# Kernel optimization log

Hardware: AMD Instinct MI355X
Metric: run time of the kernel (lower is better)

Reference implementation:

```python
import jax, jax.numpy as jnp
import numpy as np

B, S, D, E = 8, 2048, 1024, 8
TOKENS = B * S
CAPACITY = TOKENS // E  # capacity_factor=1.0, top-1 gating (deepspeed default)


def _moe_layer(x_flat, Wg, We, be):
    """DeepSpeed-style top-1 MoE: gate -> capacity drop -> dispatch -> expert GEMM -> combine.
    x_flat: [T, D]; Wg: [D, E]; We: [E, D, D]; be: [E, D]."""
    gates = jax.nn.softmax(x_flat @ Wg, axis=-1)              # [T, E]
    idx = jnp.argmax(gates, axis=1)                            # [T] expert per token
    mask = jax.nn.one_hot(idx, E, dtype=jnp.int32)             # [T, E]
    loc = jnp.cumsum(mask, axis=0) - 1                         # position within expert
    loc_s = jnp.sum(loc * mask, axis=1)                        # [T]
    keep = loc_s < CAPACITY                                    # capacity drop
    gate_s = jnp.sum(gates * mask.astype(gates.dtype), axis=1) * keep.astype(gates.dtype)
    slot = jnp.clip(loc_s, 0, CAPACITY - 1)
    # dispatch: scatter kept tokens into [E, C, D] buffer (slots are unique for kept tokens)
    disp = jnp.zeros((E, CAPACITY, D), x_flat.dtype).at[idx, slot].add(
        x_flat * keep[:, None].astype(x_flat.dtype))
    # grouped expert GEMM
    eo = jnp.einsum('ecd,edf->ecf', disp, We) + be[:, None, :]  # [E, C, D]
    # combine: gather each token's expert output, scale by its gate value
    return eo[idx, slot] * gate_s[:, None]                      # [T, D]


def reference(x, y, W1, b1, Wg2, We2, be2, Wg3, We3, be3):
    h = jnp.einsum('bsd,df->bsf', x, W1) + b1                  # dense pre-layer
    hf = h.reshape(TOKENS, D)
    o = _moe_layer(hf, Wg2, We2, be2)
    o = _moe_layer(o, Wg3, We3, be3)
    h = h + o.reshape(B, S, D)                                 # residual add
    sent = h.mean(axis=1)                                      # [B, D]
    logp = jax.nn.log_softmax(sent, axis=-1)
    return -jnp.mean(logp[jnp.arange(B), y])                   # CrossEntropyLoss


def setup_inputs() -> dict:
    key = jax.random.key(0)
    ks = jax.random.split(key, 10)
    s = 0.02
    return {
        'x': jax.random.normal(ks[0], (B, S, D), jnp.float32),
        'y': jax.random.randint(ks[1], (B,), 0, D),
        'W1': jax.random.normal(ks[2], (D, D), jnp.float32) * s,
        'b1': jnp.zeros((D,), jnp.float32),
        'Wg2': jax.random.normal(ks[3], (D, E), jnp.float32) * s,
        'We2': jax.random.normal(ks[4], (E, D, D), jnp.float32) * s,
        'be2': jnp.zeros((E, D), jnp.float32),
        'Wg3': jax.random.normal(ks[5], (D, E), jnp.float32) * s,
        'We3': jax.random.normal(ks[6], (E, D, D), jnp.float32) * s,
        'be3': jnp.zeros((E, D), jnp.float32),
    }
```

## Files before the change

### kernel.cpp

```cpp
#include <hip/hip_runtime.h>
#include <hip/hip_bf16.h>
#include <math.h>


#define TOKS 16384
#define DIM 1024
#define NEXP 8
#define CAP 2048
#define BATCH 8
#define SEQ 2048

typedef __bf16 bf16_t;
typedef __bf16 bf16x8 __attribute__((ext_vector_type(8)));
typedef float fx4 __attribute__((ext_vector_type(4)));

__device__ __forceinline__ void gll16(const bf16_t* g, bf16_t* l) {
  __builtin_amdgcn_global_load_lds(
      (const __attribute__((address_space(1))) unsigned int*)g,
      (__attribute__((address_space(3))) unsigned int*)l, 16, 0, 0);
}

__global__ __launch_bounds__(256) void k_prep_w(
    const float* __restrict__ W1, const float* __restrict__ We2,
    const float* __restrict__ We3, bf16_t* __restrict__ Wt) {
  __shared__ float t[64][65];
  const int m = blockIdx.z;
  const float* src = (m == 0) ? W1
                     : (m <= 8) ? We2 + (size_t)(m - 1) * DIM * DIM
                                : We3 + (size_t)(m - 9) * DIM * DIM;
  bf16_t* dst = Wt + (size_t)m * DIM * DIM;
  const int n0 = blockIdx.x * 64, k0 = blockIdx.y * 64;
  const int tid = threadIdx.x;
  const int r = tid >> 4, c4 = (tid & 15) * 4;
#pragma unroll
  for (int i = 0; i < 4; i++) {
    float4 v = *(const float4*)&src[(size_t)(k0 + i * 16 + r) * DIM + n0 + c4];
    t[i * 16 + r][c4] = v.x;
    t[i * 16 + r][c4 + 1] = v.y;
    t[i * 16 + r][c4 + 2] = v.z;
    t[i * 16 + r][c4 + 3] = v.w;
  }
  __syncthreads();
#pragma unroll
  for (int i = 0; i < 4; i++) {
    int rn = i * 16 + r;
    union { bf16_t b[4]; uint2 u; } tmp;
#pragma unroll
    for (int j = 0; j < 4; j++) tmp.b[j] = (bf16_t)t[c4 + j][rn];
    *(uint2*)&dst[(size_t)(n0 + rn) * DIM + k0 + c4] = tmp.u;
  }
}

__global__ __launch_bounds__(256) void k_prep_wg(
    const float* __restrict__ Wg2, const float* __restrict__ Wg3,
    bf16_t* __restrict__ WgP) {
  const int which = blockIdx.x;
  const float* src = which ? Wg3 : Wg2;
  bf16_t* dst = WgP + which * (128 * 8 * 8);
  const int tid = threadIdx.x;
#pragma unroll
  for (int j = 0; j < 4; j++) {
    int d = tid * 4 + j;
    float4 a = *(const float4*)&src[d * 8];
    float4 b = *(const float4*)&src[d * 8 + 4];
    float v[8] = {a.x, a.y, a.z, a.w, b.x, b.y, b.z, b.w};
#pragma unroll
    for (int e = 0; e < 8; e++)
      dst[((d >> 3) * 8 + e) * 8 + (d & 7)] = (bf16_t)v[e];
  }
}

__global__ __launch_bounds__(256) void k_cvt_x(const float* __restrict__ x,
                                               bf16_t* __restrict__ xb) {
  size_t i = ((size_t)blockIdx.x * 256 + threadIdx.x) * 8;
  float4 a = *(const float4*)&x[i];
  float4 b = *(const float4*)&x[i + 4];
  union { bf16_t h[8]; uint4 u; } t;
  t.h[0] = (bf16_t)a.x; t.h[1] = (bf16_t)a.y; t.h[2] = (bf16_t)a.z; t.h[3] = (bf16_t)a.w;
  t.h[4] = (bf16_t)b.x; t.h[5] = (bf16_t)b.y; t.h[6] = (bf16_t)b.z; t.h[7] = (bf16_t)b.w;
  *(uint4*)&xb[i] = t.u;
}

__global__ __launch_bounds__(256) void k_gemm_dense(
    const bf16_t* __restrict__ A, const bf16_t* __restrict__ Bt,
    const float* __restrict__ bias, bf16_t* __restrict__ out) {
  __shared__ alignas(16) bf16_t As[128 * 64];
  __shared__ alignas(16) bf16_t Bs[128 * 64];
  const int tid = threadIdx.x;
  const int lane = tid & 63, wave = tid >> 6;
  const int quad = lane >> 4, l15 = lane & 15;
  const int wr = (wave >> 1) * 64, wc = (wave & 1) * 64;
  const int id = blockIdx.x;
  const int j_ = id >> 3;
  const int m0 = ((id & 7) * 16 + (j_ >> 3)) * 128;
  const int n0 = (j_ & 7) * 128;
  const int kc = (tid & 7) ^ ((tid >> 3) & 7);
  const int rbase = tid >> 3;

  const bf16_t* gA[4];
  const bf16_t* gB[4];
  bf16_t* lA[4];
  bf16_t* lB[4];
#pragma unroll
  for (int i = 0; i < 4; i++) {
    int r = rbase + 32 * i;
    gA[i] = A + (size_t)(m0 + r) * DIM + kc * 8;
    gB[i] = Bt + (size_t)(n0 + r) * DIM + kc * 8;
    lA[i] = &As[(wave * 64 + 256 * i) * 8];
    lB[i] = &Bs[(wave * 64 + 256 * i) * 8];
  }

  fx4 acc[4][4];
#pragma unroll
  for (int i = 0; i < 4; i++)
#pragma unroll
    for (int j = 0; j < 4; j++) acc[i][j] = (fx4)0.0f;

  for (int k0 = 0; k0 < DIM; k0 += 64) {
#pragma unroll
    for (int i = 0; i < 4; i++) gll16(gA[i] + k0, lA[i]);
#pragma unroll
    for (int i = 0; i < 4; i++) gll16(gB[i] + k0, lB[i]);
    __syncthreads();
#pragma unroll
    for (int s = 0; s < 2; s++) {
      const int pofs = ((s * 4 + quad) ^ (l15 & 7)) << 3;
      bf16x8 av[4], bv[4];
#pragma unroll
      for (int i = 0; i < 4; i++)
        av[i] = *(const bf16x8*)&As[(wr + i * 16 + l15) * 64 + pofs];
#pragma unroll
      for (int j = 0; j < 4; j++)
        bv[j] = *(const bf16x8*)&Bs[(wc + j * 16 + l15) * 64 + pofs];
#pragma unroll
      for (int i = 0; i < 4; i++)
#pragma unroll
        for (int j = 0; j < 4; j++)
          acc[i][j] = __builtin_amdgcn_mfma_f32_16x16x32_bf16(av[i], bv[j], acc[i][j], 0, 0, 0);
    }
    __syncthreads();
  }
#pragma unroll
  for (int j = 0; j < 4; j++) {
    int col = n0 + wc + j * 16 + l15;
    float bb = bias[col];
#pragma unroll
    for (int i = 0; i < 4; i++)
#pragma unroll
      for (int r = 0; r < 4; r++) {
        int m = m0 + wr + i * 16 + quad * 4 + r;
        out[(size_t)m * DIM + col] = (bf16_t)(acc[i][j][r] + bb);
      }
  }
}

__global__ __launch_bounds__(256) void k_gate_mm(
    const bf16_t* __restrict__ act, const bf16_t* __restrict__ WgP,
    int* __restrict__ idx, float* __restrict__ gate) {
  __shared__ alignas(16) bf16_t As[64 * 64];
  __shared__ alignas(16) bf16_t WgS[128 * 64];
  __shared__ float L[64][8];
  const int tid = threadIdx.x;
  const int lane = tid & 63, wave = tid >> 6;
  const int quad = lane >> 4, l15 = lane & 15;
  const int m0 = blockIdx.x * 64;
  const int kc = (tid & 7) ^ ((tid >> 3) & 7);
  const int rbase = tid >> 3;

#pragma unroll
  for (int j = 0; j < 4; j++)
    gll16(WgP + (j * 256 + wave * 64 + lane) * 8,
          &WgS[(j * 256 + wave * 64) * 8]);

  const bf16_t* gA[2];
  bf16_t* lA[2];
#pragma unroll
  for (int i = 0; i < 2; i++) {
    gA[i] = act + (size_t)(m0 + rbase + 32 * i) * DIM + kc * 8;
    lA[i] = &As[wave * 512 + i * 2048];
  }

  fx4 acc = (fx4)0.0f;
  for (int k0 = 0; k0 < DIM; k0 += 64) {
#pragma unroll
    for (int i = 0; i < 2; i++) gll16(gA[i] + k0, lA[i]);
    __syncthreads();
#pragma unroll
    for (int s = 0; s < 2; s++) {
      const int pofs = ((s * 4 + quad) ^ (l15 & 7)) << 3;
      bf16x8 av = *(const bf16x8*)&As[(wave * 16 + l15) * 64 + pofs];
      bf16x8 bv = *(const bf16x8*)&WgS[((k0 >> 3) + s * 4 + quad) * 64 + (l15 & 7) * 8];
      acc = __builtin_amdgcn_mfma_f32_16x16x32_bf16(av, bv, acc, 0, 0, 0);
    }
    __syncthreads();
  }
  if (l15 < 8) {
#pragma unroll
    for (int r = 0; r < 4; r++) L[wave * 16 + quad * 4 + r][l15] = acc[r];
  }
  __syncthreads();
  if (tid < 64) {
    float lg[8];
#pragma unroll
    for (int e = 0; e < 8; e++) lg[e] = L[tid][e];
    float best = lg[0];
    int bi = 0;
#pragma unroll
    for (int e = 1; e < 8; e++)
      if (lg[e] > best) { best = lg[e]; bi = e; }
    float s = 0.f;
#pragma unroll
    for (int e = 0; e < 8; e++) s += expf(lg[e] - best);
    idx[m0 + tid] = bi;
    gate[m0 + tid] = 1.0f / s;
  }
}

__global__ __launch_bounds__(1024) void k_route(
    const int* __restrict__ idx, int* __restrict__ tok, int* __restrict__ cnt,
    int* __restrict__ drop, int* __restrict__ ndrop) {
  const int e = blockIdx.x;
  const int tid = threadIdx.x, lane = tid & 63, wv = tid >> 6;
  __shared__ int wsum[16];
  const int4* p = (const int4*)(idx + tid * 16);
  int m[16];
  int c = 0;
#pragma unroll
  for (int j = 0; j < 4; j++) {
    int4 v = p[j];
    m[j * 4 + 0] = (v.x == e);
    m[j * 4 + 1] = (v.y == e);
    m[j * 4 + 2] = (v.z == e);
    m[j * 4 + 3] = (v.w == e);
    c += m[j * 4] + m[j * 4 + 1] + m[j * 4 + 2] + m[j * 4 + 3];
  }
  int sc = c;
#pragma unroll
  for (int off = 1; off < 64; off <<= 1) {
    int n = __shfl_up(sc, off);
    if (lane >= off) sc += n;
  }
  if (lane == 63) wsum[wv] = sc;
  __syncthreads();
  int wb = 0, tot = 0;
#pragma unroll
  for (int i = 0; i < 16; i++) {
    int s = wsum[i];
    tot += s;
    if (i < wv) wb += s;
  }
  int pos = wb + sc - c;
#pragma unroll
  for (int j = 0; j < 16; j++) {
    if (m[j]) {
      if (pos < CAP) {
        tok[e * CAP + pos] = tid * 16 + j;
      } else {
        int di = atomicAdd(ndrop, 1);
        drop[di] = tid * 16 + j;
      }
      pos++;
    }
  }
  if (tid == 0) cnt[e] = tot < CAP ? tot : CAP;
}

__global__ __launch_bounds__(128) void k_zero_rows(
    bf16_t* __restrict__ buf, const int* __restrict__ drop,
    const int* __restrict__ ndrop) {
  const int nd = *ndrop;
  const uint4 z = {0u, 0u, 0u, 0u};
  for (int j = blockIdx.x; j < nd; j += gridDim.x) {
    int t = drop[j];
    ((uint4*)(buf + (size_t)t * DIM))[threadIdx.x] = z;
  }
}

__global__ __launch_bounds__(256) void k_gemm_expert(
    const bf16_t* __restrict__ Ain, const bf16_t* __restrict__ Wt,
    const float* __restrict__ be, const int* __restrict__ tok,
    const int* __restrict__ cnt, const float* __restrict__ gate,
    const bf16_t* __restrict__ zp, bf16_t* __restrict__ outp) {
  const int id = blockIdx.x;
  const int e = id & 7;
  const int j_ = id >> 3;
  const int c0 = (j_ >> 3) * 128;
  const int n0 = (j_ & 7) * 128;
  const int count = cnt[e];
  if (c0 >= count) return;
  const bf16_t* Bt = Wt + (size_t)e * DIM * DIM;
  const float* bias = be + (size_t)e * DIM;
  const int* tk = tok + e * CAP;

  __shared__ alignas(16) bf16_t As[128 * 64];
  __shared__ alignas(16) bf16_t Bs[128 * 64];
  const int tid = threadIdx.x;
  const int lane = tid & 63, wave = tid >> 6;
  const int quad = lane >> 4, l15 = lane & 15;
  const int wr = (wave >> 1) * 64, wc = (wave & 1) * 64;
  const int kc = (tid & 7) ^ ((tid >> 3) & 7);
  const int rbase = tid >> 3;

  const bf16_t* gA[4];
  const bf16_t* gB[4];
  bf16_t* lA[4];
  bf16_t* lB[4];
#pragma unroll
  for (int i = 0; i < 4; i++) {
    int r = rbase + 32 * i;
    int ca = c0 + r;
    gA[i] = (ca < count) ? Ain + (size_t)tk[ca] * DIM + kc * 8 : zp;
    gB[i] = Bt + (size_t)(n0 + r) * DIM + kc * 8;
    lA[i] = &As[(wave * 64 + 256 * i) * 8];
    lB[i] = &Bs[(wave * 64 + 256 * i) * 8];
  }

  fx4 acc[4][4];
#pragma unroll
  for (int i = 0; i < 4; i++)
#pragma unroll
    for (int j = 0; j < 4; j++) acc[i][j] = (fx4)0.0f;

  for (int k0 = 0; k0 < DIM; k0 += 64) {
#pragma unroll
    for (int i = 0; i < 4; i++) gll16(gA[i] + k0, lA[i]);
#pragma unroll
    for (int i = 0; i < 4; i++) gll16(gB[i] + k0, lB[i]);
    __syncthreads();
#pragma unroll
    for (int s = 0; s < 2; s++) {
      const int pofs = ((s * 4 + quad) ^ (l15 & 7)) << 3;
      bf16x8 av[4], bv[4];
#pragma unroll
      for (int i = 0; i < 4; i++)
        av[i] = *(const bf16x8*)&As[(wr + i * 16 + l15) * 64 + pofs];
#pragma unroll
      for (int j = 0; j < 4; j++)
        bv[j] = *(const bf16x8*)&Bs[(wc + j * 16 + l15) * 64 + pofs];
#pragma unroll
      for (int i = 0; i < 4; i++)
#pragma unroll
        for (int j = 0; j < 4; j++)
          acc[i][j] = __builtin_amdgcn_mfma_f32_16x16x32_bf16(av[i], bv[j], acc[i][j], 0, 0, 0);
    }
    __syncthreads();
  }
#pragma unroll
  for (int i = 0; i < 4; i++)
#pragma unroll
    for (int r = 0; r < 4; r++) {
      int c = c0 + wr + i * 16 + quad * 4 + r;
      if (c < count) {
        int t = tk[c];
        float g = gate[t];
#pragma unroll
        for (int j = 0; j < 4; j++) {
          int col = n0 + wc + j * 16 + l15;
          outp[(size_t)t * DIM + col] = (bf16_t)((acc[i][j][r] + bias[col]) * g);
        }
      }
    }
}

__global__ __launch_bounds__(256) void k_reduce_sent(
    const bf16_t* __restrict__ h, const bf16_t* __restrict__ o2,
    float* __restrict__ sent) {
  const int tid = threadIdx.x;
  const int d8 = (tid & 127) * 8;
  const int sg = tid >> 7;
  const int b = blockIdx.y;
  const int s0 = blockIdx.x * 64 + sg * 32;
  float acc[8] = {0.f, 0.f, 0.f, 0.f, 0.f, 0.f, 0.f, 0.f};
  const size_t base = ((size_t)b * SEQ + s0) * DIM + d8;
  for (int i = 0; i < 32; i++) {
    union { bf16_t v[8]; uint4 u; } hh, oo;
    hh.u = *(const uint4*)&h[base + (size_t)i * DIM];
    oo.u = *(const uint4*)&o2[base + (size_t)i * DIM];
#pragma unroll
    for (int j = 0; j < 8; j++) acc[j] += (float)hh.v[j] + (float)oo.v[j];
  }
#pragma unroll
  for (int j = 0; j < 8; j++)
    atomicAdd(&sent[b * DIM + d8 + j], acc[j] * (1.0f / SEQ));
}

__global__ __launch_bounds__(256) void k_loss(
    const float* __restrict__ sent, const int* __restrict__ y,
    float* __restrict__ out) {
  const int b = blockIdx.x, tid = threadIdx.x;
  const float* sb = sent + b * DIM;
  __shared__ float red[256];
  float m = -1e30f;
  for (int d = tid; d < DIM; d += 256) m = fmaxf(m, sb[d]);
  red[tid] = m;
  __syncthreads();
  for (int s = 128; s; s >>= 1) {
    if (tid < s) red[tid] = fmaxf(red[tid], red[tid + s]);
    __syncthreads();
  }
  m = red[0];
  __syncthreads();
  float sum = 0.f;
  for (int d = tid; d < DIM; d += 256) sum += expf(sb[d] - m);
  red[tid] = sum;
  __syncthreads();
  for (int s = 128; s; s >>= 1) {
    if (tid < s) red[tid] += red[tid + s];
    __syncthreads();
  }
  if (tid == 0) atomicAdd(out, (m + logf(red[0]) - sb[y[b]]) * (1.0f / BATCH));
}

extern "C" void kernel_launch(void* const* d_in, const int* in_sizes, int n_in,
                              void* d_out, int out_size, void* d_ws, size_t ws_size,
                              hipStream_t stream) {
  (void)in_sizes; (void)n_in; (void)out_size; (void)ws_size;
  const float* x   = (const float*)d_in[0];
  const int*   y   = (const int*)d_in[1];
  const float* W1  = (const float*)d_in[2];
  const float* b1  = (const float*)d_in[3];
  const float* Wg2 = (const float*)d_in[4];
  const float* We2 = (const float*)d_in[5];
  const float* be2 = (const float*)d_in[6];
  const float* Wg3 = (const float*)d_in[7];
  const float* We3 = (const float*)d_in[8];
  const float* be3 = (const float*)d_in[9];

  char* p = (char*)d_ws;
  size_t off = 0;
  auto carve = [&](size_t bytes) -> char* {
    char* r = p + off;
    off += (bytes + 255) & ~(size_t)255;
    return r;
  };
  bf16_t* Wt   = (bf16_t*)carve((size_t)17 * DIM * DIM * 2);
  bf16_t* WgP  = (bf16_t*)carve(2 * 128 * 8 * 8 * 2);
  bf16_t* h    = (bf16_t*)carve((size_t)TOKS * DIM * 2);
  bf16_t* o1   = (bf16_t*)carve((size_t)TOKS * DIM * 2);
  bf16_t* o2   = (bf16_t*)carve((size_t)TOKS * DIM * 2);
  int*    idx  = (int*)carve(TOKS * 4);
  float*  gate = (float*)carve(TOKS * 4);
  int*    tok  = (int*)carve(NEXP * CAP * 4);
  int*    cnt  = (int*)carve(NEXP * 4);
  int*    drop2 = (int*)carve(TOKS * 4);
  int*    drop3 = (int*)carve(TOKS * 4);
  size_t zoff0 = off;
  float*  sent = (float*)carve(BATCH * DIM * 4);
  bf16_t* zp   = (bf16_t*)carve(4096);
  int*    nd2  = (int*)carve(256);
  int*    nd3  = (int*)carve(256);
  size_t zbytes = off - zoff0;
  bf16_t* xb   = o2;

  hipMemsetAsync(sent, 0, zbytes, stream);
  hipMemsetAsync(d_out, 0, 4, stream);

  k_prep_w<<<dim3(16, 16, 17), 256, 0, stream>>>(W1, We2, We3, Wt);
  k_prep_wg<<<2, 256, 0, stream>>>(Wg2, Wg3, WgP);
  k_cvt_x<<<TOKS * DIM / 8 / 256, 256, 0, stream>>>(x, xb);

  k_gemm_dense<<<(TOKS / 128) * (DIM / 128), 256, 0, stream>>>(xb, Wt, b1, h);

  k_gate_mm<<<TOKS / 64, 256, 0, stream>>>(h, WgP, idx, gate);
  k_route<<<NEXP, 1024, 0, stream>>>(idx, tok, cnt, drop2, nd2);
  k_zero_rows<<<256, 128, 0, stream>>>(o1, drop2, nd2);
  k_gemm_expert<<<NEXP * (CAP / 128) * (DIM / 128), 256, 0, stream>>>(
      h, Wt + (size_t)1 * DIM * DIM, be2, tok, cnt, gate, zp, o1);

  k_gate_mm<<<TOKS / 64, 256, 0, stream>>>(o1, WgP + 128 * 8 * 8, idx, gate);
  k_route<<<NEXP, 1024, 0, stream>>>(idx, tok, cnt, drop3, nd3);
  k_zero_rows<<<256, 128, 0, stream>>>(o2, drop3, nd3);
  k_gemm_expert<<<NEXP * (CAP / 128) * (DIM / 128), 256, 0, stream>>>(
      o1, Wt + (size_t)9 * DIM * DIM, be3, tok, cnt, gate, zp, o2);

  k_reduce_sent<<<dim3(SEQ / 64, BATCH), 256, 0, stream>>>(h, o2, sent);
  k_loss<<<BATCH, 256, 0, stream>>>(sent, y, (float*)d_out);
}
```

Before: 398.9 us.

## Fuse gating logits, sentence sums and drop-zeroing into GEMM epilogues

Merges the three prep kernels into one launch. The dense GEMM epilogue now stages h in shared memory and computes partial gate logits and the h sentence sums there, accumulating with atomics. The first expert GEMM computes the next layer's logits the same way. Routing now does argmax and softmax itself and zeroes dropped rows, which removes the separate gate_mm and zero_rows kernels and the rereads of h and o1. The cost is extra atomics, larger shared memory use in the GEMMs, and gate logits that now come from bf16-rounded activations summed in fp32 partials.

```diff
diff --git a/kernel.cpp b/kernel.cpp
--- a/kernel.cpp
+++ b/kernel.cpp
@@ -20,72 +20,78 @@
       (__attribute__((address_space(3))) unsigned int*)l, 16, 0, 0);
 }
 
-__global__ __launch_bounds__(256) void k_prep_w(
+#define PW_BLOCKS (17 * 256)
+#define CVT_BLOCKS (TOKS * DIM / 8 / 256)
+__global__ __launch_bounds__(256) void k_prep(
     const float* __restrict__ W1, const float* __restrict__ We2,
-    const float* __restrict__ We3, bf16_t* __restrict__ Wt) {
-  __shared__ float t[64][65];
-  const int m = blockIdx.z;
-  const float* src = (m == 0) ? W1
-                     : (m <= 8) ? We2 + (size_t)(m - 1) * DIM * DIM
-                                : We3 + (size_t)(m - 9) * DIM * DIM;
-  bf16_t* dst = Wt + (size_t)m * DIM * DIM;
-  const int n0 = blockIdx.x * 64, k0 = blockIdx.y * 64;
+    const float* __restrict__ We3, const float* __restrict__ Wg2,
+    const float* __restrict__ Wg3, const float* __restrict__ x,
+    bf16_t* __restrict__ Wt, bf16_t* __restrict__ WgP,
+    bf16_t* __restrict__ xb) {
+  const int id = blockIdx.x;
   const int tid = threadIdx.x;
-  const int r = tid >> 4, c4 = (tid & 15) * 4;
-#pragma unroll
-  for (int i = 0; i < 4; i++) {
-    float4 v = *(const float4*)&src[(size_t)(k0 + i * 16 + r) * DIM + n0 + c4];
-    t[i * 16 + r][c4] = v.x;
-    t[i * 16 + r][c4 + 1] = v.y;
-    t[i * 16 + r][c4 + 2] = v.z;
-    t[i * 16 + r][c4 + 3] = v.w;
-  }
-  __syncthreads();
-#pragma unroll
-  for (int i = 0; i < 4; i++) {
-    int rn = i * 16 + r;
-    union { bf16_t b[4]; uint2 u; } tmp;
-#pragma unroll
-    for (int j = 0; j < 4; j++) tmp.b[j] = (bf16_t)t[c4 + j][rn];
-    *(uint2*)&dst[(size_t)(n0 + rn) * DIM + k0 + c4] = tmp.u;
-  }
-}
-
-__global__ __launch_bounds__(256) void k_prep_wg(
-    const float* __restrict__ Wg2, const float* __restrict__ Wg3,
-    bf16_t* __restrict__ WgP) {
-  const int which = blockIdx.x;
-  const float* src = which ? Wg3 : Wg2;
-  bf16_t* dst = WgP + which * (128 * 8 * 8);
-  const int tid = threadIdx.x;
-#pragma unroll
-  for (int j = 0; j < 4; j++) {
-    int d = tid * 4 + j;
-    float4 a = *(const float4*)&src[d * 8];
-    float4 b = *(const float4*)&src[d * 8 + 4];
-    float v[8] = {a.x, a.y, a.z, a.w, b.x, b.y, b.z, b.w};
-#pragma unroll
-    for (int e = 0; e < 8; e++)
-      dst[((d >> 3) * 8 + e) * 8 + (d & 7)] = (bf16_t)v[e];
-  }
-}
-
-__global__ __launch_bounds__(256) void k_cvt_x(const float* __restrict__ x,
-                                               bf16_t* __restrict__ xb) {
-  size_t i = ((size_t)blockIdx.x * 256 + threadIdx.x) * 8;
-  float4 a = *(const float4*)&x[i];
-  float4 b = *(const float4*)&x[i + 4];
-  union { bf16_t h[8]; uint4 u; } t;
-  t.h[0] = (bf16_t)a.x; t.h[1] = (bf16_t)a.y; t.h[2] = (bf16_t)a.z; t.h[3] = (bf16_t)a.w;
-  t.h[4] = (bf16_t)b.x; t.h[5] = (bf16_t)b.y; t.h[6] = (bf16_t)b.z; t.h[7] = (bf16_t)b.w;
-  *(uint4*)&xb[i] = t.u;
-}
-
+  if (id < PW_BLOCKS) {
+    __shared__ float t[64][65];
+    const int m = id >> 8, rem = id & 255;
+    const int n0 = (rem & 15) * 64, k0 = (rem >> 4) * 64;
+    const float* src = (m == 0) ? W1
+                       : (m <= 8) ? We2 + (size_t)(m - 1) * DIM * DIM
+                                  : We3 + (size_t)(m - 9) * DIM * DIM;
+    bf16_t* dst = Wt + (size_t)m * DIM * DIM;
+    const int r = tid >> 4, c4 = (tid & 15) * 4;
+#pragma unroll
+    for (int i = 0; i < 4; i++) {
+      float4 v = *(const float4*)&src[(size_t)(k0 + i * 16 + r) * DIM + n0 + c4];
+      t[i * 16 + r][c4] = v.x;
+      t[i * 16 + r][c4 + 1] = v.y;
+      t[i * 16 + r][c4 + 2] = v.z;
+      t[i * 16 + r][c4 + 3] = v.w;
+    }
+    __syncthreads();
+#pragma unroll
+    for (int i = 0; i < 4; i++) {
+      int rn = i * 16 + r;
+      union { bf16_t b[4]; uint2 u; } tmp;
+#pragma unroll
+      for (int j = 0; j < 4; j++) tmp.b[j] = (bf16_t)t[c4 + j][rn];
+      *(uint2*)&dst[(size_t)(n0 + rn) * DIM + k0 + c4] = tmp.u;
+    }
+  } else if (id < PW_BLOCKS + 2) {
+    const int which = id - PW_BLOCKS;
+    const float* src = which ? Wg3 : Wg2;
+    bf16_t* dst = WgP + which * (128 * 8 * 8);
+#pragma unroll
+    for (int j = 0; j < 4; j++) {
+      int d = tid * 4 + j;
+      float4 a = *(const float4*)&src[d * 8];
+      float4 b = *(const float4*)&src[d * 8 + 4];
+      float v[8] = {a.x, a.y, a.z, a.w, b.x, b.y, b.z, b.w};
+#pragma unroll
+      for (int e = 0; e < 8; e++)
+        dst[((d >> 3) * 8 + e) * 8 + (d & 7)] = (bf16_t)v[e];
+    }
+  } else {
+    const int cid = id - PW_BLOCKS - 2;
+    size_t i = ((size_t)cid * 256 + tid) * 8;
+    float4 a = *(const float4*)&x[i];
+    float4 b = *(const float4*)&x[i + 4];
+    union { bf16_t h[8]; uint4 u; } t;
+    t.h[0] = (bf16_t)a.x; t.h[1] = (bf16_t)a.y; t.h[2] = (bf16_t)a.z; t.h[3] = (bf16_t)a.w;
+    t.h[4] = (bf16_t)b.x; t.h[5] = (bf16_t)b.y; t.h[6] = (bf16_t)b.z; t.h[7] = (bf16_t)b.w;
+    *(uint4*)&xb[i] = t.u;
+  }
+}
+
+#define HSTRIDE 136
 __global__ __launch_bounds__(256) void k_gemm_dense(
     const bf16_t* __restrict__ A, const bf16_t* __restrict__ Bt,
-    const float* __restrict__ bias, bf16_t* __restrict__ out) {
-  __shared__ alignas(16) bf16_t As[128 * 64];
-  __shared__ alignas(16) bf16_t Bs[128 * 64];
+    const float* __restrict__ bias, const bf16_t* __restrict__ WgP2,
+    bf16_t* __restrict__ out, float* __restrict__ logits,
+    float* __restrict__ sent) {
+  __shared__ alignas(16) bf16_t smem[128 * HSTRIDE];
+  __shared__ alignas(16) bf16_t WgN[1024];
+  bf16_t* As = smem;
+  bf16_t* Bs = smem + 128 * 64;
   const int tid = threadIdx.x;
   const int lane = tid & 63, wave = tid >> 6;
   const int quad = lane >> 4, l15 = lane & 15;
@@ -97,6 +103,11 @@
   const int kc = (tid & 7) ^ ((tid >> 3) & 7);
   const int rbase = tid >> 3;
 
+  if (wave == 0) {
+    gll16(WgP2 + n0 * 8 + lane * 8, WgN);
+    gll16(WgP2 + n0 * 8 + 512 + lane * 8, WgN + 512);
+  }
+
   const bf16_t* gA[4];
   const bf16_t* gB[4];
   bf16_t* lA[4];
@@ -140,99 +151,76 @@
     }
     __syncthreads();
   }
+  bf16_t* hs = smem;
 #pragma unroll
   for (int j = 0; j < 4; j++) {
-    int col = n0 + wc + j * 16 + l15;
-    float bb = bias[col];
+    int colL = wc + j * 16 + l15;
+    float bb = bias[n0 + colL];
 #pragma unroll
     for (int i = 0; i < 4; i++)
 #pragma unroll
       for (int r = 0; r < 4; r++) {
-        int m = m0 + wr + i * 16 + quad * 4 + r;
-        out[(size_t)m * DIM + col] = (bf16_t)(acc[i][j][r] + bb);
+        int rowL = wr + i * 16 + quad * 4 + r;
+        bf16_t hv = (bf16_t)(acc[i][j][r] + bb);
+        out[(size_t)(m0 + rowL) * DIM + n0 + colL] = hv;
+        hs[rowL * HSTRIDE + colL] = hv;
       }
   }
-}
-
-__global__ __launch_bounds__(256) void k_gate_mm(
-    const bf16_t* __restrict__ act, const bf16_t* __restrict__ WgP,
-    int* __restrict__ idx, float* __restrict__ gate) {
-  __shared__ alignas(16) bf16_t As[64 * 64];
-  __shared__ alignas(16) bf16_t WgS[128 * 64];
-  __shared__ float L[64][8];
-  const int tid = threadIdx.x;
-  const int lane = tid & 63, wave = tid >> 6;
-  const int quad = lane >> 4, l15 = lane & 15;
-  const int m0 = blockIdx.x * 64;
-  const int kc = (tid & 7) ^ ((tid >> 3) & 7);
-  const int rbase = tid >> 3;
-
-#pragma unroll
-  for (int j = 0; j < 4; j++)
-    gll16(WgP + (j * 256 + wave * 64 + lane) * 8,
-          &WgS[(j * 256 + wave * 64) * 8]);
-
-  const bf16_t* gA[2];
-  bf16_t* lA[2];
-#pragma unroll
-  for (int i = 0; i < 2; i++) {
-    gA[i] = act + (size_t)(m0 + rbase + 32 * i) * DIM + kc * 8;
-    lA[i] = &As[wave * 512 + i * 2048];
-  }
-
-  fx4 acc = (fx4)0.0f;
-  for (int k0 = 0; k0 < DIM; k0 += 64) {
-#pragma unroll
-    for (int i = 0; i < 2; i++) gll16(gA[i] + k0, lA[i]);
-    __syncthreads();
-#pragma unroll
-    for (int s = 0; s < 2; s++) {
-      const int pofs = ((s * 4 + quad) ^ (l15 & 7)) << 3;
-      bf16x8 av = *(const bf16x8*)&As[(wave * 16 + l15) * 64 + pofs];
-      bf16x8 bv = *(const bf16x8*)&WgS[((k0 >> 3) + s * 4 + quad) * 64 + (l15 & 7) * 8];
-      acc = __builtin_amdgcn_mfma_f32_16x16x32_bf16(av, bv, acc, 0, 0, 0);
-    }
-    __syncthreads();
+  __syncthreads();
+  fx4 lac0 = (fx4)0.0f, lac1 = (fx4)0.0f;
+#pragma unroll
+  for (int ks = 0; ks < 4; ks++) {
+    bf16x8 bv = *(const bf16x8*)&WgN[((ks * 4 + quad) * 8 + (l15 & 7)) * 8];
+    bf16x8 av0 = *(const bf16x8*)&hs[(wave * 32 + l15) * HSTRIDE + ks * 32 + quad * 8];
+    bf16x8 av1 = *(const bf16x8*)&hs[(wave * 32 + 16 + l15) * HSTRIDE + ks * 32 + quad * 8];
+    lac0 = __builtin_amdgcn_mfma_f32_16x16x32_bf16(av0, bv, lac0, 0, 0, 0);
+    lac1 = __builtin_amdgcn_mfma_f32_16x16x32_bf16(av1, bv, lac1, 0, 0, 0);
   }
   if (l15 < 8) {
 #pragma unroll
-    for (int r = 0; r < 4; r++) L[wave * 16 + quad * 4 + r][l15] = acc[r];
-  }
-  __syncthreads();
-  if (tid < 64) {
-    float lg[8];
-#pragma unroll
-    for (int e = 0; e < 8; e++) lg[e] = L[tid][e];
-    float best = lg[0];
-    int bi = 0;
-#pragma unroll
-    for (int e = 1; e < 8; e++)
-      if (lg[e] > best) { best = lg[e]; bi = e; }
-    float s = 0.f;
-#pragma unroll
-    for (int e = 0; e < 8; e++) s += expf(lg[e] - best);
-    idx[m0 + tid] = bi;
-    gate[m0 + tid] = 1.0f / s;
+    for (int r = 0; r < 4; r++) {
+      atomicAdd(&logits[(m0 + wave * 32 + quad * 4 + r) * 8 + l15], lac0[r]);
+      atomicAdd(&logits[(m0 + wave * 32 + 16 + quad * 4 + r) * 8 + l15], lac1[r]);
+    }
+  }
+  {
+    const int colL = tid & 127, rg = tid >> 7;
+    float ss = 0.f;
+#pragma unroll 8
+    for (int rr = 0; rr < 64; rr++) ss += (float)hs[(rg * 64 + rr) * HSTRIDE + colL];
+    atomicAdd(&sent[(m0 >> 11) * DIM + n0 + colL], ss * (1.0f / SEQ));
   }
 }
 
 __global__ __launch_bounds__(1024) void k_route(
-    const int* __restrict__ idx, int* __restrict__ tok, int* __restrict__ cnt,
-    int* __restrict__ drop, int* __restrict__ ndrop) {
+    const float* __restrict__ logits, int* __restrict__ tok,
+    int* __restrict__ cnt, float* __restrict__ gate,
+    bf16_t* __restrict__ obuf) {
   const int e = blockIdx.x;
   const int tid = threadIdx.x, lane = tid & 63, wv = tid >> 6;
   __shared__ int wsum[16];
-  const int4* p = (const int4*)(idx + tid * 16);
+  __shared__ int dlist[2048];
   int m[16];
   int c = 0;
 #pragma unroll
-  for (int j = 0; j < 4; j++) {
-    int4 v = p[j];
-    m[j * 4 + 0] = (v.x == e);
-    m[j * 4 + 1] = (v.y == e);
-    m[j * 4 + 2] = (v.z == e);
-    m[j * 4 + 3] = (v.w == e);
-    c += m[j * 4] + m[j * 4 + 1] + m[j * 4 + 2] + m[j * 4 + 3];
+  for (int j = 0; j < 16; j++) {
+    int t = tid * 16 + j;
+    const float* lp = logits + t * 8;
+    float4 a = *(const float4*)lp, b = *(const float4*)(lp + 4);
+    float l[8] = {a.x, a.y, a.z, a.w, b.x, b.y, b.z, b.w};
+    float best = l[0];
+    int bi = 0;
+#pragma unroll
+    for (int k = 1; k < 8; k++)
+      if (l[k] > best) { best = l[k]; bi = k; }
+    m[j] = (bi == e);
+    if (m[j]) {
+      float s = 0.f;
+#pragma unroll
+      for (int k = 0; k < 8; k++) s += expf(l[k] - best);
+      gate[t] = 1.0f / s;
+      c++;
+    }
   }
   int sc = c;
 #pragma unroll
@@ -250,37 +238,40 @@
     if (i < wv) wb += s;
   }
   int pos = wb + sc - c;
+  const uint4 z = {0u, 0u, 0u, 0u};
 #pragma unroll
   for (int j = 0; j < 16; j++) {
     if (m[j]) {
+      int t = tid * 16 + j;
       if (pos < CAP) {
-        tok[e * CAP + pos] = tid * 16 + j;
+        tok[e * CAP + pos] = t;
       } else {
-        int di = atomicAdd(ndrop, 1);
-        drop[di] = tid * 16 + j;
+        int di = pos - CAP;
+        if (di < 2048) dlist[di] = t;
+        else
+          for (int k = 0; k < 128; k++) *(uint4*)&obuf[(size_t)t * DIM + k * 8] = z;
       }
       pos++;
     }
   }
   if (tid == 0) cnt[e] = tot < CAP ? tot : CAP;
-}
-
-__global__ __launch_bounds__(128) void k_zero_rows(
-    bf16_t* __restrict__ buf, const int* __restrict__ drop,
-    const int* __restrict__ ndrop) {
-  const int nd = *ndrop;
-  const uint4 z = {0u, 0u, 0u, 0u};
-  for (int j = blockIdx.x; j < nd; j += gridDim.x) {
-    int t = drop[j];
-    ((uint4*)(buf + (size_t)t * DIM))[threadIdx.x] = z;
-  }
-}
-
+  __syncthreads();
+  int ndl = tot - CAP;
+  ndl = ndl < 0 ? 0 : (ndl > 2048 ? 2048 : ndl);
+  const int grp = tid >> 7, li = tid & 127;
+  for (int d = grp; d < ndl; d += 8) {
+    int t = dlist[d];
+    *(uint4*)&obuf[(size_t)t * DIM + li * 8] = z;
+  }
+}
+
+template <bool FG>
 __global__ __launch_bounds__(256) void k_gemm_expert(
     const bf16_t* __restrict__ Ain, const bf16_t* __restrict__ Wt,
     const float* __restrict__ be, const int* __restrict__ tok,
     const int* __restrict__ cnt, const float* __restrict__ gate,
-    const bf16_t* __restrict__ zp, bf16_t* __restrict__ outp) {
+    const bf16_t* __restrict__ zp, bf16_t* __restrict__ outp,
+    const bf16_t* __restrict__ WgPn, float* __restrict__ logits) {
   const int id = blockIdx.x;
   const int e = id & 7;
   const int j_ = id >> 3;
@@ -292,14 +283,21 @@
   const float* bias = be + (size_t)e * DIM;
   const int* tk = tok + e * CAP;
 
-  __shared__ alignas(16) bf16_t As[128 * 64];
-  __shared__ alignas(16) bf16_t Bs[128 * 64];
+  __shared__ alignas(16) bf16_t smem[128 * HSTRIDE];
+  __shared__ alignas(16) bf16_t WgN[1024];
+  bf16_t* As = smem;
+  bf16_t* Bs = smem + 128 * 64;
   const int tid = threadIdx.x;
   const int lane = tid & 63, wave = tid >> 6;
   const int quad = lane >> 4, l15 = lane & 15;
   const int wr = (wave >> 1) * 64, wc = (wave & 1) * 64;
   const int kc = (tid & 7) ^ ((tid >> 3) & 7);
   const int rbase = tid >> 3;
+
+  if (FG && wave == 0) {
+    gll16(WgPn + n0 * 8 + lane * 8, WgN);
+    gll16(WgPn + n0 * 8 + 512 + lane * 8, WgN + 512);
+  }
 
   const bf16_t* gA[4];
   const bf16_t* gB[4];
@@ -345,26 +343,51 @@
     }
     __syncthreads();
   }
+  bf16_t* hs = smem;
 #pragma unroll
   for (int i = 0; i < 4; i++)
 #pragma unroll
     for (int r = 0; r < 4; r++) {
-      int c = c0 + wr + i * 16 + quad * 4 + r;
-      if (c < count) {
-        int t = tk[c];
-        float g = gate[t];
-#pragma unroll
-        for (int j = 0; j < 4; j++) {
-          int col = n0 + wc + j * 16 + l15;
-          outp[(size_t)t * DIM + col] = (bf16_t)((acc[i][j][r] + bias[col]) * g);
-        }
+      int rowL = wr + i * 16 + quad * 4 + r;
+      int c = c0 + rowL;
+      bool ok = c < count;
+      int t = 0;
+      float g = 0.f;
+      if (ok) { t = tk[c]; g = gate[t]; }
+#pragma unroll
+      for (int j = 0; j < 4; j++) {
+        int colL = wc + j * 16 + l15;
+        float v = ok ? (acc[i][j][r] + bias[n0 + colL]) * g : 0.f;
+        bf16_t vb = (bf16_t)v;
+        if (FG) hs[rowL * HSTRIDE + colL] = vb;
+        if (ok) outp[(size_t)t * DIM + n0 + colL] = vb;
       }
     }
-}
-
-__global__ __launch_bounds__(256) void k_reduce_sent(
-    const bf16_t* __restrict__ h, const bf16_t* __restrict__ o2,
-    float* __restrict__ sent) {
+  if (FG) {
+    __syncthreads();
+    fx4 lac0 = (fx4)0.0f, lac1 = (fx4)0.0f;
+#pragma unroll
+    for (int ks = 0; ks < 4; ks++) {
+      bf16x8 bv = *(const bf16x8*)&WgN[((ks * 4 + quad) * 8 + (l15 & 7)) * 8];
+      bf16x8 av0 = *(const bf16x8*)&hs[(wave * 32 + l15) * HSTRIDE + ks * 32 + quad * 8];
+      bf16x8 av1 = *(const bf16x8*)&hs[(wave * 32 + 16 + l15) * HSTRIDE + ks * 32 + quad * 8];
+      lac0 = __builtin_amdgcn_mfma_f32_16x16x32_bf16(av0, bv, lac0, 0, 0, 0);
+      lac1 = __builtin_amdgcn_mfma_f32_16x16x32_bf16(av1, bv, lac1, 0, 0, 0);
+    }
+    if (l15 < 8) {
+#pragma unroll
+      for (int r = 0; r < 4; r++) {
+        int ca = c0 + wave * 32 + quad * 4 + r;
+        int cb = ca + 16;
+        if (ca < count) atomicAdd(&logits[tk[ca] * 8 + l15], lac0[r]);
+        if (cb < count) atomicAdd(&logits[tk[cb] * 8 + l15], lac1[r]);
+      }
+    }
+  }
+}
+
+__global__ __launch_bounds__(256) void k_reduce_o2(
+    const bf16_t* __restrict__ o2, float* __restrict__ sent) {
   const int tid = threadIdx.x;
   const int d8 = (tid & 127) * 8;
   const int sg = tid >> 7;
@@ -373,11 +396,10 @@
   float acc[8] = {0.f, 0.f, 0.f, 0.f, 0.f, 0.f, 0.f, 0.f};
   const size_t base = ((size_t)b * SEQ + s0) * DIM + d8;
   for (int i = 0; i < 32; i++) {
-    union { bf16_t v[8]; uint4 u; } hh, oo;
-    hh.u = *(const uint4*)&h[base + (size_t)i * DIM];
+    union { bf16_t v[8]; uint4 u; } oo;
     oo.u = *(const uint4*)&o2[base + (size_t)i * DIM];
 #pragma unroll
-    for (int j = 0; j < 8; j++) acc[j] += (float)hh.v[j] + (float)oo.v[j];
+    for (int j = 0; j < 8; j++) acc[j] += (float)oo.v[j];
   }
 #pragma unroll
   for (int j = 0; j < 8; j++)
@@ -438,41 +460,36 @@
   bf16_t* h    = (bf16_t*)carve((size_t)TOKS * DIM * 2);
   bf16_t* o1   = (bf16_t*)carve((size_t)TOKS * DIM * 2);
   bf16_t* o2   = (bf16_t*)carve((size_t)TOKS * DIM * 2);
-  int*    idx  = (int*)carve(TOKS * 4);
   float*  gate = (float*)carve(TOKS * 4);
   int*    tok  = (int*)carve(NEXP * CAP * 4);
   int*    cnt  = (int*)carve(NEXP * 4);
-  int*    drop2 = (int*)carve(TOKS * 4);
-  int*    drop3 = (int*)carve(TOKS * 4);
   size_t zoff0 = off;
   float*  sent = (float*)carve(BATCH * DIM * 4);
   bf16_t* zp   = (bf16_t*)carve(4096);
-  int*    nd2  = (int*)carve(256);
-  int*    nd3  = (int*)carve(256);
+  float*  lg2  = (float*)carve(TOKS * 8 * 4);
+  float*  lg3  = (float*)carve(TOKS * 8 * 4);
   size_t zbytes = off - zoff0;
   bf16_t* xb   = o2;
 
   hipMemsetAsync(sent, 0, zbytes, stream);
   hipMemsetAsync(d_out, 0, 4, stream);
 
-  k_prep_w<<<dim3(16, 16, 17), 256, 0, stream>>>(W1, We2, We3, Wt);
-  k_prep_wg<<<2, 256, 0, stream>>>(Wg2, Wg3, WgP);
-  k_cvt_x<<<TOKS * DIM / 8 / 256, 256, 0, stream>>>(x, xb);
-
-  k_gemm_dense<<<(TOKS / 128) * (DIM / 128), 256, 0, stream>>>(xb, Wt, b1, h);
-
-  k_gate_mm<<<TOKS / 64, 256, 0, stream>>>(h, WgP, idx, gate);
-  k_route<<<NEXP, 1024, 0, stream>>>(idx, tok, cnt, drop2, nd2);
-  k_zero_rows<<<256, 128, 0, stream>>>(o1, drop2, nd2);
-  k_gemm_expert<<<NEXP * (CAP / 128) * (DIM / 128), 256, 0, stream>>>(
-      h, Wt + (size_t)1 * DIM * DIM, be2, tok, cnt, gate, zp, o1);
-
-  k_gate_mm<<<TOKS / 64, 256, 0, stream>>>(o1, WgP + 128 * 8 * 8, idx, gate);
-  k_route<<<NEXP, 1024, 0, stream>>>(idx, tok, cnt, drop3, nd3);
-  k_zero_rows<<<256, 128, 0, stream>>>(o2, drop3, nd3);
-  k_gemm_expert<<<NEXP * (CAP / 128) * (DIM / 128), 256, 0, stream>>>(
-      o1, Wt + (size_t)9 * DIM * DIM, be3, tok, cnt, gate, zp, o2);
-
-  k_reduce_sent<<<dim3(SEQ / 64, BATCH), 256, 0, stream>>>(h, o2, sent);
+  k_prep<<<PW_BLOCKS + 2 + CVT_BLOCKS, 256, 0, stream>>>(
+      W1, We2, We3, Wg2, Wg3, x, Wt, WgP, xb);
+
+  k_gemm_dense<<<(TOKS / 128) * (DIM / 128), 256, 0, stream>>>(
+      xb, Wt, b1, WgP, h, lg2, sent);
+
+  k_route<<<NEXP, 1024, 0, stream>>>(lg2, tok, cnt, gate, o1);
+  k_gemm_expert<true><<<NEXP * (CAP / 128) * (DIM / 128), 256, 0, stream>>>(
+      h, Wt + (size_t)1 * DIM * DIM, be2, tok, cnt, gate, zp, o1,
+      WgP + 128 * 8 * 8, lg3);
+
+  k_route<<<NEXP, 1024, 0, stream>>>(lg3, tok, cnt, gate, o2);
+  k_gemm_expert<false><<<NEXP * (CAP / 128) * (DIM / 128), 256, 0, stream>>>(
+      o1, Wt + (size_t)9 * DIM * DIM, be3, tok, cnt, gate, zp, o2,
+      nullptr, nullptr);
+
+  k_reduce_o2<<<dim3(SEQ / 64, BATCH), 256, 0, stream>>>(o2, sent);
   k_loss<<<BATCH, 256, 0, stream>>>(sent, y, (float*)d_out);
 }
```

New measurement: 439.8 us. 10.3% more time.
